# Kernel tuning notes

Hardware: AMD Instinct MI355X
Metric: run time of the kernel (lower is better)

## Reference

```python
import jax, jax.numpy as jnp
import numpy as np

N_NODES = 50000
N_EDGES = 1_600_000
T = 2
F_IN = 128
F_OUT = 128


def setup_inputs() -> dict:
    key = jax.random.key(0)
    k1, k2, k3, k4, k5, k6 = jax.random.split(key, 6)
    node_features = jax.random.normal(k1, (N_NODES, T, F_IN), dtype=jnp.float32)
    edge_weights = jax.random.uniform(k2, (T, N_EDGES), dtype=jnp.float32)
    src = jax.random.randint(k3, (N_EDGES,), 0, N_NODES, dtype=jnp.int32)
    dst = jax.random.randint(k4, (N_EDGES,), 0, N_NODES, dtype=jnp.int32)
    W = jax.random.normal(k5, (F_OUT, F_IN), dtype=jnp.float32) / np.sqrt(F_IN)
    b = jax.random.normal(k6, (F_OUT,), dtype=jnp.float32) * 0.01
    return {"node_features": node_features, "edge_weights": edge_weights,
            "src": src, "dst": dst, "W": W, "b": b}


def reference(node_features, edge_weights, src, dst, W, b):
    # DGL: graph.edata['e'] = edge_weights.t().unsqueeze(-1)  -> [E, T, 1]
    w = jnp.transpose(edge_weights)[:, :, None]          # [E, T, 1]
    # u_mul_e: gather src node features, scale by edge weight -> [E, T, F]
    msg = node_features[src] * w
    # sum aggregation at destination nodes -> [N, T, F]
    h = jax.ops.segment_sum(msg, dst, num_segments=node_features.shape[0])
    # Linear(in_features, out_features) with bias
    return jnp.einsum('ntf,of->nto', h, W) + b
```

## Files before the change

kernel.cpp:

```cpp
#include <hip/hip_runtime.h>
#include <hip/hip_bf16.h>
#include <hip/hip_fp16.h>


#define TBLOCK 256
#define CAP 64
#define NGRP 8
#define GSH 5
#define GSZ (1 << GSH)
#define NQ 1563
#define BCAP 224
#define APB 1536

typedef _Float16 half8 __attribute__((ext_vector_type(8)));
typedef float    f32x4 __attribute__((ext_vector_type(4)));
typedef float    float4_v __attribute__((ext_vector_type(4)));

__device__ __forceinline__ void do_append(
        const int* __restrict__ src, const int* __restrict__ dst,
        const float* __restrict__ ew, int* __restrict__ qcnt,
        unsigned long long* __restrict__ buckets, int E, int ablk) {
    const int g = ablk & (NGRP - 1);
    int* qc = qcnt + (size_t)g * NQ;
    unsigned long long* bk = buckets + (size_t)g * NQ * BCAP;

    const int idx = ablk * TBLOCK + (int)threadIdx.x;
    const int stride = APB * TBLOCK * 4;

    for (int e4 = idx * 4; e4 < E; e4 += stride) {
        if (e4 + 3 < E) {
            int4   d4  = *(const int4*)&dst[e4];
            int4   s4  = *(const int4*)&src[e4];
            float4 w04 = *(const float4*)&ew[e4];
            float4 w14 = *(const float4*)&ew[(size_t)E + e4];
            const int   dd[4] = {d4.x, d4.y, d4.z, d4.w};
            const int   ss[4] = {s4.x, s4.y, s4.z, s4.w};
            const float w0[4] = {w04.x, w04.y, w04.z, w04.w};
            const float w1[4] = {w14.x, w14.y, w14.z, w14.w};
            #pragma unroll
            for (int k = 0; k < 4; ++k) {
                int d = dd[k];
                int q = d >> GSH, dloc = d & (GSZ - 1);
                int pos = atomicAdd(&qc[q], 1);
                if (pos < BCAP) {
                    __half2 hw = __floats2half2_rn(w0[k], w1[k]);
                    bk[(size_t)q * BCAP + pos] =
                        (unsigned long long)(unsigned)(ss[k] | (dloc << 16)) |
                        ((unsigned long long)(*(unsigned*)&hw) << 32);
                }
            }
        } else {
            for (int e = e4; e < E; ++e) {
                int d = dst[e];
                int q = d >> GSH, dloc = d & (GSZ - 1);
                int pos = atomicAdd(&qc[q], 1);
                if (pos < BCAP) {
                    __half2 hw = __floats2half2_rn(ew[e], ew[(size_t)E + e]);
                    bk[(size_t)q * BCAP + pos] =
                        (unsigned long long)(unsigned)(src[e] | (dloc << 16)) |
                        ((unsigned long long)(*(unsigned*)&hw) << 32);
                }
            }
        }
    }
}

__device__ __forceinline__ void do_transform(
        const float* __restrict__ x, const float* __restrict__ W,
        __half* __restrict__ y, int nrows, int blk) {
    __shared__ _Float16 Wl[128 * 128];
    __shared__ _Float16 xl[64 * 128];

    const int tid = threadIdx.x;
    const int rowbase = blk * 64;

    for (int p = tid; p < 2048; p += TBLOCK) {
        int o = p >> 4, ch = p & 15;
        const float4* g = (const float4*)&W[(size_t)o * 128 + ch * 8];
        float4 u0 = g[0], u1 = g[1];
        half8 h;
        h[0] = (_Float16)u0.x; h[1] = (_Float16)u0.y;
        h[2] = (_Float16)u0.z; h[3] = (_Float16)u0.w;
        h[4] = (_Float16)u1.x; h[5] = (_Float16)u1.y;
        h[6] = (_Float16)u1.z; h[7] = (_Float16)u1.w;
        *(half8*)&Wl[o * 128 + ((ch ^ (o & 7)) << 3)] = h;
    }
    for (int p = tid; p < 1024; p += TBLOCK) {
        int r = p >> 4, ch = p & 15;
        int row = rowbase + r;
        half8 h = {};
        if (row < nrows) {
            const float4* g = (const float4*)&x[(size_t)row * 128 + ch * 8];
            float4 u0 = g[0], u1 = g[1];
            h[0] = (_Float16)u0.x; h[1] = (_Float16)u0.y;
            h[2] = (_Float16)u0.z; h[3] = (_Float16)u0.w;
            h[4] = (_Float16)u1.x; h[5] = (_Float16)u1.y;
            h[6] = (_Float16)u1.z; h[7] = (_Float16)u1.w;
        }
        *(half8*)&xl[r * 128 + ((ch ^ (r & 7)) << 3)] = h;
    }
    __syncthreads();

    const int l    = tid & 63;
    const int wv   = tid >> 6;
    const int rloc = wv * 16 + (l & 15);
    const int kg   = (l >> 4);

    half8 xf[4];
    #pragma unroll
    for (int s = 0; s < 4; ++s)
        xf[s] = *(const half8*)&xl[rloc * 128 + (((s * 4 + kg) ^ (rloc & 7)) << 3)];

    f32x4 acc[8] = {};
    #pragma unroll
    for (int s = 0; s < 4; ++s) {
        #pragma unroll
        for (int c = 0; c < 8; ++c) {
            int o = c * 16 + (l & 15);
            half8 wf = *(const half8*)&Wl[o * 128 + (((s * 4 + kg) ^ (o & 7)) << 3)];
            acc[c] = __builtin_amdgcn_mfma_f32_16x16x32_f16(wf, xf[s], acc[c], 0, 0, 0);
        }
    }

    const int row = rowbase + rloc;
    if (row < nrows) {
        #pragma unroll
        for (int c = 0; c < 8; ++c) {
            __half2 h0 = __floats2half2_rn(acc[c][0], acc[c][1]);
            __half2 h1 = __floats2half2_rn(acc[c][2], acc[c][3]);
            uint2 pk;
            pk.x = *(unsigned*)&h0;
            pk.y = *(unsigned*)&h1;
            *(uint2*)&y[(size_t)row * 128 + c * 16 + kg * 4] = pk;
        }
    }
}

__global__ void __launch_bounds__(TBLOCK)
fused_kernel(const float* __restrict__ x, const float* __restrict__ W,
             __half* __restrict__ y,
             const int* __restrict__ src, const int* __restrict__ dst,
             const float* __restrict__ ew, int* __restrict__ qcnt,
             unsigned long long* __restrict__ buckets,
             int nrows, int E) {
    if ((int)blockIdx.x < APB)
        do_append(src, dst, ew, qcnt, buckets, E, blockIdx.x);
    else
        do_transform(x, W, y, nrows, blockIdx.x - APB);
}

__global__ void __launch_bounds__(TBLOCK)
pull2_kernel(const __half* __restrict__ y, const int* __restrict__ qcnt,
             const unsigned long long* __restrict__ buckets,
             const float* __restrict__ b, float* __restrict__ out, int N) {
    __shared__ int lcnt[GSZ];
    __shared__ unsigned long long lent[GSZ * CAP];

    const int q = blockIdx.x;
    const int tid = threadIdx.x;
    if (tid < GSZ) lcnt[tid] = 0;
    __syncthreads();

    #pragma unroll 1
    for (int g = 0; g < NGRP; ++g) {
        int c = qcnt[(size_t)g * NQ + q];
        if (c > BCAP) c = BCAP;
        const unsigned long long* bk = buckets + ((size_t)g * NQ + q) * BCAP;
        for (int i = tid; i < c; i += TBLOCK) {
            unsigned long long ent = bk[i];
            int dloc = (int)((ent >> 16) & (GSZ - 1));
            int pos = atomicAdd(&lcnt[dloc], 1);
            if (pos < CAP) lent[dloc * CAP + pos] = ent;
        }
    }
    __syncthreads();

    const int wv   = __builtin_amdgcn_readfirstlane(tid >> 6);
    const int lane = tid & 63;
    const bool hi  = lane >= 32;
    const uint2* yv = (const uint2*)y;
    const float4 bv = ((const float4*)b)[lane & 31];

    #define ACCUM(ee, rr) do {                                            \
        unsigned wbits = (unsigned)((ee) >> 32);                          \
        __half2 w2 = *(__half2*)&wbits;                                   \
        float aw = __half2float(hi ? __high2half(w2) : __low2half(w2));   \
        float2 f0 = __half22float2(*(const __half2*)&(rr).x);             \
        float2 f1 = __half22float2(*(const __half2*)&(rr).y);             \
        acc.x += aw * f0.x; acc.y += aw * f0.y;                           \
        acc.z += aw * f1.x; acc.w += aw * f1.y; } while (0)

    #pragma unroll 1
    for (int j = 0; j < GSZ / 4; ++j) {
        const int n = wv * (GSZ / 4) + j;
        const int node = q * GSZ + n;
        if (node >= N) break;
        int c = lcnt[n];
        if (c > CAP) c = CAP;
        const unsigned long long* lp = &lent[n * CAP];
        float4 acc = bv;
        int i = 0;
        for (; i + 3 < c; i += 4) {
            unsigned long long e0 = lp[i], e1 = lp[i + 1];
            unsigned long long e2 = lp[i + 2], e3 = lp[i + 3];
            uint2 r0 = yv[(size_t)(e0 & 0xFFFFu) * 64 + lane];
            uint2 r1 = yv[(size_t)(e1 & 0xFFFFu) * 64 + lane];
            uint2 r2 = yv[(size_t)(e2 & 0xFFFFu) * 64 + lane];
            uint2 r3 = yv[(size_t)(e3 & 0xFFFFu) * 64 + lane];
            ACCUM(e0, r0); ACCUM(e1, r1); ACCUM(e2, r2); ACCUM(e3, r3);
        }
        for (; i < c; ++i) {
            unsigned long long e0 = lp[i];
            uint2 r0 = yv[(size_t)(e0 & 0xFFFFu) * 64 + lane];
            ACCUM(e0, r0);
        }
        float4_v av; av.x = acc.x; av.y = acc.y; av.z = acc.z; av.w = acc.w;
        __builtin_nontemporal_store(
            av, (float4_v*)&((float4*)out)[(size_t)node * 64 + lane]);
    }
}

extern "C" void kernel_launch(void* const* d_in, const int* in_sizes, int n_in,
                              void* d_out, int out_size, void* d_ws, size_t ws_size,
                              hipStream_t stream) {
    const float* x   = (const float*)d_in[0];
    const float* ew  = (const float*)d_in[1];
    const int*   src = (const int*)d_in[2];
    const int*   dst = (const int*)d_in[3];
    const float* W   = (const float*)d_in[4];
    const float* b   = (const float*)d_in[5];
    float* out = (float*)d_out;

    const int E     = in_sizes[2];
    const int nrows = in_sizes[0] / 128;
    const int N     = nrows / 2;

    char* w8 = (char*)d_ws;
    __half* y  = (__half*)w8;  w8 += (size_t)nrows * 128 * sizeof(__half);
    int* qcnt  = (int*)w8;     w8 += (size_t)NGRP * NQ * sizeof(int);
    w8 = (char*)(((uintptr_t)w8 + 15) & ~(uintptr_t)15);
    unsigned long long* buckets = (unsigned long long*)w8;

    (void)hipMemsetAsync(qcnt, 0, (size_t)NGRP * NQ * sizeof(int), stream);

    const int TT = (nrows + 63) / 64;
    fused_kernel<<<APB + TT, TBLOCK, 0, stream>>>(
        x, W, y, src, dst, ew, qcnt, buckets, nrows, E);

    pull2_kernel<<<NQ, TBLOCK, 0, stream>>>(y, qcnt, buckets, b, out, N);
}
```

Baseline: 216.8 us.

## Pre-pack W into MFMA fragment layout and drop LDS staging in transform

A new prep kernel converts W to fp16 once, stores it in the exact per-lane MFMA fragment order, and zeroes the bucket counters, which replaces the memset. The transform blocks then read x rows and W fragments straight from global memory into registers, with no shared-memory staging and no __syncthreads. Previously every transform block reconverted all of W to fp16 and used 48KB of LDS, which limited occupancy. The cost is an extra small kernel launch and uncoalesced per-lane global loads of W fragments, which rely on L2 caching.

```diff
diff --git a/kernel.cpp b/kernel.cpp
--- a/kernel.cpp
+++ b/kernel.cpp
@@ -15,6 +15,22 @@
 typedef _Float16 half8 __attribute__((ext_vector_type(8)));
 typedef float    f32x4 __attribute__((ext_vector_type(4)));
 typedef float    float4_v __attribute__((ext_vector_type(4)));
+
+__global__ void __launch_bounds__(TBLOCK)
+prep_kernel(const float* __restrict__ W, _Float16* __restrict__ Wfrag,
+            int* __restrict__ qcnt, int qtotal) {
+    int i = blockIdx.x * TBLOCK + threadIdx.x;
+    if (i < 128 * 128) {
+        int j  = i & 7;
+        int r  = (i >> 3) & 15;
+        int q  = i >> 7;
+        int kg = q & 3;
+        int s  = (q >> 2) & 3;
+        int c  = q >> 4;
+        Wfrag[i] = (_Float16)W[(size_t)(c * 16 + r) * 128 + s * 32 + kg * 8 + j];
+    }
+    if (i < qtotal) qcnt[i] = 0;
+}
 
 __device__ __forceinline__ void do_append(
         const int* __restrict__ src, const int* __restrict__ dst,
@@ -66,64 +82,42 @@
 }
 
 __device__ __forceinline__ void do_transform(
-        const float* __restrict__ x, const float* __restrict__ W,
+        const float* __restrict__ x, const _Float16* __restrict__ Wfrag,
         __half* __restrict__ y, int nrows, int blk) {
-    __shared__ _Float16 Wl[128 * 128];
-    __shared__ _Float16 xl[64 * 128];
-
     const int tid = threadIdx.x;
-    const int rowbase = blk * 64;
-
-    for (int p = tid; p < 2048; p += TBLOCK) {
-        int o = p >> 4, ch = p & 15;
-        const float4* g = (const float4*)&W[(size_t)o * 128 + ch * 8];
-        float4 u0 = g[0], u1 = g[1];
+    const int l   = tid & 63;
+    const int wv  = tid >> 6;
+    const int r15 = l & 15;
+    const int kg  = l >> 4;
+    const int row = blk * 64 + wv * 16 + r15;
+    const bool ok = row < nrows;
+
+    const float* xrow = x + (size_t)(ok ? row : 0) * 128;
+
+    half8 xf[4];
+    #pragma unroll
+    for (int s = 0; s < 4; ++s) {
+        float4 u0 = *(const float4*)&xrow[s * 32 + kg * 8];
+        float4 u1 = *(const float4*)&xrow[s * 32 + kg * 8 + 4];
         half8 h;
         h[0] = (_Float16)u0.x; h[1] = (_Float16)u0.y;
         h[2] = (_Float16)u0.z; h[3] = (_Float16)u0.w;
         h[4] = (_Float16)u1.x; h[5] = (_Float16)u1.y;
         h[6] = (_Float16)u1.z; h[7] = (_Float16)u1.w;
-        *(half8*)&Wl[o * 128 + ((ch ^ (o & 7)) << 3)] = h;
-    }
-    for (int p = tid; p < 1024; p += TBLOCK) {
-        int r = p >> 4, ch = p & 15;
-        int row = rowbase + r;
-        half8 h = {};
-        if (row < nrows) {
-            const float4* g = (const float4*)&x[(size_t)row * 128 + ch * 8];
-            float4 u0 = g[0], u1 = g[1];
-            h[0] = (_Float16)u0.x; h[1] = (_Float16)u0.y;
-            h[2] = (_Float16)u0.z; h[3] = (_Float16)u0.w;
-            h[4] = (_Float16)u1.x; h[5] = (_Float16)u1.y;
-            h[6] = (_Float16)u1.z; h[7] = (_Float16)u1.w;
-        }
-        *(half8*)&xl[r * 128 + ((ch ^ (r & 7)) << 3)] = h;
-    }
-    __syncthreads();
-
-    const int l    = tid & 63;
-    const int wv   = tid >> 6;
-    const int rloc = wv * 16 + (l & 15);
-    const int kg   = (l >> 4);
-
-    half8 xf[4];
-    #pragma unroll
-    for (int s = 0; s < 4; ++s)
-        xf[s] = *(const half8*)&xl[rloc * 128 + (((s * 4 + kg) ^ (rloc & 7)) << 3)];
+        xf[s] = h;
+    }
 
     f32x4 acc[8] = {};
     #pragma unroll
     for (int s = 0; s < 4; ++s) {
         #pragma unroll
         for (int c = 0; c < 8; ++c) {
-            int o = c * 16 + (l & 15);
-            half8 wf = *(const half8*)&Wl[o * 128 + (((s * 4 + kg) ^ (o & 7)) << 3)];
+            half8 wf = *(const half8*)&Wfrag[(size_t)(c * 16 + s * 4 + kg) * 128 + r15 * 8];
             acc[c] = __builtin_amdgcn_mfma_f32_16x16x32_f16(wf, xf[s], acc[c], 0, 0, 0);
         }
     }
 
-    const int row = rowbase + rloc;
-    if (row < nrows) {
+    if (ok) {
         #pragma unroll
         for (int c = 0; c < 8; ++c) {
             __half2 h0 = __floats2half2_rn(acc[c][0], acc[c][1]);
@@ -137,7 +131,7 @@
 }
 
 __global__ void __launch_bounds__(TBLOCK)
-fused_kernel(const float* __restrict__ x, const float* __restrict__ W,
+fused_kernel(const float* __restrict__ x, const _Float16* __restrict__ Wfrag,
              __half* __restrict__ y,
              const int* __restrict__ src, const int* __restrict__ dst,
              const float* __restrict__ ew, int* __restrict__ qcnt,
@@ -146,7 +140,7 @@
     if ((int)blockIdx.x < APB)
         do_append(src, dst, ew, qcnt, buckets, E, blockIdx.x);
     else
-        do_transform(x, W, y, nrows, blockIdx.x - APB);
+        do_transform(x, Wfrag, y, nrows, blockIdx.x - APB);
 }
 
 __global__ void __launch_bounds__(TBLOCK)
@@ -236,16 +230,17 @@
     const int N     = nrows / 2;
 
     char* w8 = (char*)d_ws;
-    __half* y  = (__half*)w8;  w8 += (size_t)nrows * 128 * sizeof(__half);
-    int* qcnt  = (int*)w8;     w8 += (size_t)NGRP * NQ * sizeof(int);
+    __half* y  = (__half*)w8;      w8 += (size_t)nrows * 128 * sizeof(__half);
+    int* qcnt  = (int*)w8;         w8 += (size_t)NGRP * NQ * sizeof(int);
+    _Float16* Wfrag = (_Float16*)w8;  w8 += 128 * 128 * sizeof(_Float16);
     w8 = (char*)(((uintptr_t)w8 + 15) & ~(uintptr_t)15);
     unsigned long long* buckets = (unsigned long long*)w8;
 
-    (void)hipMemsetAsync(qcnt, 0, (size_t)NGRP * NQ * sizeof(int), stream);
+    prep_kernel<<<64, TBLOCK, 0, stream>>>(W, Wfrag, qcnt, NGRP * NQ);
 
     const int TT = (nrows + 63) / 64;
     fused_kernel<<<APB + TT, TBLOCK, 0, stream>>>(
-        x, W, y, src, dst, ew, qcnt, buckets, nrows, E);
+        x, Wfrag, y, src, dst, ew, qcnt, buckets, nrows, E);
 
     pull2_kernel<<<NQ, TBLOCK, 0, stream>>>(y, qcnt, buckets, b, out, N);
 }
```

After: 230.1 us. 1.06x slower.
